# Kernel optimization log

Measured on AMD Instinct MI355X. Metric: run time of the kernel, lower is better.

## Reference

```python
import jax, jax.numpy as jnp
import numpy as np

B = 1024          # number of sessions (graphs)
D = 128           # emb_dim
NH = 4            # num_heads
VOCAB = 50000     # POI vocabulary
NDIST = 512       # distance buckets
MAX_LEN = 160     # max session length


def _lengths():
    # deterministic variable session lengths in [64, 160]
    return np.asarray(64 + (np.arange(B) % 97), dtype=np.int64)


def _layernorm(x, g, b, eps=1e-8):
    mu = x.mean(-1, keepdims=True)
    var = ((x - mu) ** 2).mean(-1, keepdims=True)
    return (x - mu) / jnp.sqrt(var + eps) * g + b


def setup_inputs() -> dict:
    key = jax.random.key(0)
    ks = jax.random.split(key, 16)
    lengths = _lengths()
    N = int(lengths.sum())
    # node -> (graph id, position within graph)
    batch_ids = np.repeat(np.arange(B), lengths)
    node_pos = np.concatenate([np.arange(l) for l in lengths])
    # consecutive (sequence) edges within each session
    starts = np.concatenate([[0], np.cumsum(lengths)[:-1]])
    src = np.concatenate([s + np.arange(l - 1) for s, l in zip(starts, lengths)])
    dst = src + 1
    edge_index = np.stack([src, dst]).astype(np.int64)
    E = edge_index.shape[1]
    s = 1.0 / np.sqrt(D)
    return {
        "POI_embs": jax.random.normal(ks[0], (VOCAB, D), jnp.float32) * 0.02,
        "delta_dis_embs": jax.random.normal(ks[1], (NDIST, D), jnp.float32) * 0.02,
        "att_W": jax.random.normal(ks[2], (D, D), jnp.float32) * s,
        "a_src": jax.random.normal(ks[3], (D,), jnp.float32) * 0.1,
        "a_dst": jax.random.normal(ks[4], (D,), jnp.float32) * 0.1,
        "in_proj_w": jax.random.normal(ks[5], (3 * D, D), jnp.float32) * s,
        "in_proj_b": jnp.zeros((3 * D,), jnp.float32),
        "out_proj_w": jax.random.normal(ks[6], (D, D), jnp.float32) * s,
        "out_proj_b": jnp.zeros((D,), jnp.float32),
        "ln1_g": jnp.ones((D,), jnp.float32), "ln1_b": jnp.zeros((D,), jnp.float32),
        "ln2_g": jnp.ones((D,), jnp.float32), "ln2_b": jnp.zeros((D,), jnp.float32),
        "ffn_w1": jax.random.normal(ks[7], (D, D), jnp.float32) * s,
        "ffn_b1": jnp.zeros((D,), jnp.float32),
        "ffn_w2": jax.random.normal(ks[8], (D, D), jnp.float32) * s,
        "ffn_b2": jnp.zeros((D,), jnp.float32),
        "sess_idx": jax.random.randint(ks[9], (N,), 0, VOCAB),
        "edge_dist": jax.random.randint(ks[10], (E,), 0, NDIST),
        "edge_index": jnp.asarray(edge_index),
        "batch_ids": jnp.asarray(batch_ids),
        "node_pos": jnp.asarray(node_pos),
        "lengths": jnp.asarray(lengths),
    }


def reference(POI_embs, delta_dis_embs, att_W, a_src, a_dst,
              in_proj_w, in_proj_b, out_proj_w, out_proj_b,
              ln1_g, ln1_b, ln2_g, ln2_b,
              ffn_w1, ffn_b1, ffn_w2, ffn_b2,
              sess_idx, edge_dist, edge_index, batch_ids, node_pos, lengths):
    N = sess_idx.shape[0]
    E = edge_index.shape[1]
    # ---- BiSeqGCN: gather -> attention logits -> scatter-softmax -> scatter-add
    x = POI_embs[sess_idx]                    # [N, D] node features
    edge_l = delta_dis_embs[edge_dist]        # [E, D] edge features
    src, dst = edge_index[0], edge_index[1]
    # bidirectional edges: forward (src->dst) then reversed (dst->src)
    j = jnp.concatenate([src, dst])           # message source  x_j
    i = jnp.concatenate([dst, src])           # message target  x_i
    x_i = x[i]                                # [2E, D]
    x_j = x[j]                                # [2E, D]
    fwd_coeff = (x_i[:E] + edge_l) @ att_W.T  # [E, D]
    bwd_coeff = x_i[E:] @ att_W.T             # [E, D]
    logits = jnp.concatenate([fwd_coeff @ a_src, bwd_coeff @ a_dst])  # [2E]
    # scatter-softmax over destination node (torch_geometric softmax, eps=1e-16)
    m = jax.ops.segment_max(logits, i, num_segments=N)
    e = jnp.exp(logits - m[i])
    ssum = jax.ops.segment_sum(e, i, num_segments=N)
    attn = e / (ssum[i] + 1e-16)
    H_u = jax.ops.segment_sum(x_j * attn[:, None], i, num_segments=N)  # [N, D]
    # ---- split/pad to [B, Lmax, D] + padding mask
    Bn = lengths.shape[0]
    pad = jnp.zeros((Bn, MAX_LEN, D), H_u.dtype).at[batch_ids, node_pos].set(H_u)
    mask = jnp.arange(MAX_LEN)[None, :] < lengths[:, None]  # [B, Lmax]
    # ---- MultiheadAttention (Q = LayerNorm(pad); K = V = pad)
    Q = _layernorm(pad, ln1_g, ln1_b)
    Wq, Wk, Wv = jnp.split(in_proj_w, 3, axis=0)
    bq, bk, bv = jnp.split(in_proj_b, 3)
    hd = D // NH
    q = (Q @ Wq.T + bq).reshape(Bn, MAX_LEN, NH, hd)
    k = (pad @ Wk.T + bk).reshape(Bn, MAX_LEN, NH, hd)
    v = (pad @ Wv.T + bv).reshape(Bn, MAX_LEN, NH, hd)
    scores = jnp.einsum('bqhd,bkhd->bhqk', q, k) / jnp.sqrt(jnp.asarray(hd, q.dtype))
    scores = jnp.where(mask[:, None, None, :], scores, -jnp.inf)
    w = jax.nn.softmax(scores, axis=-1)
    ctx = jnp.einsum('bhqk,bkhd->bqhd', w, v).reshape(Bn, MAX_LEN, D)
    out = ctx @ out_proj_w.T + out_proj_b
    out = out + Q
    out = _layernorm(out, ln2_g, ln2_b)
    # ---- PFFN (1x1 convs == per-token linears) with residual
    ffn = jax.nn.relu(out @ ffn_w1.T + ffn_b1) @ ffn_w2.T + ffn_b2
    out = out + ffn
    # ---- masked mean pool over valid positions
    mf = mask[..., None].astype(out.dtype)
    S_u = (out * mf).sum(axis=1) / lengths[:, None].astype(out.dtype)
    return S_u
```

## Files before the change

### kernel.cpp

```cpp
#include <hip/hip_runtime.h>
#include <float.h>


#define D 128
#define NHEAD 4
#define HD 32
#define MAXL 160
#define MAXNK 10
#define VP 168
#define WP 136

typedef __attribute__((ext_vector_type(8))) short short8;
typedef __attribute__((ext_vector_type(4))) float floatx4;

__device__ __forceinline__ float lo2f(unsigned u) {
    union { unsigned i; float f; } x; x.i = u << 16; return x.f;
}
__device__ __forceinline__ float hi2f(unsigned u) {
    union { unsigned i; float f; } x; x.i = u & 0xffff0000u; return x.f;
}
__device__ __forceinline__ unsigned pack2(float a, float b) {
    unsigned r;
    asm("v_cvt_pk_bf16_f32 %0, %1, %2" : "=v"(r) : "v"(a), "v"(b));
    return r;
}
__device__ __forceinline__ unsigned short f2bf(float f) {
    return (unsigned short)pack2(f, 0.f);
}
__device__ __forceinline__ unsigned short f2bfi(float f) {
    union { float f; unsigned i; } x; x.f = f;
    unsigned r = x.i + 0x7fffu + ((x.i >> 16) & 1u);
    return (unsigned short)(r >> 16);
}
__device__ __forceinline__ unsigned pack2i(float a, float b) {
    return (unsigned)f2bfi(a) | ((unsigned)f2bfi(b) << 16);
}
__device__ __forceinline__ float bf2f(unsigned short u) {
    union { unsigned i; float f; } x; x.i = (unsigned)u << 16; return x.f;
}

__launch_bounds__(128)
__global__ void prep1(const float* __restrict__ att_W, const float* __restrict__ a_src,
                      const float* __restrict__ a_dst, const float* __restrict__ in_proj_w,
                      const float* __restrict__ in_proj_b, const float* __restrict__ g1,
                      const float* __restrict__ b1, float* __restrict__ c_src,
                      float* __restrict__ c_dst, float* __restrict__ u, float* __restrict__ z) {
    int p = blockIdx.x;
    int q = threadIdx.x;
    __shared__ float red[4][2];
    float w  = att_W[q * D + p];
    float wq = in_proj_w[p * D + q];
    float s  = a_src[q] * w;
    float d  = a_dst[q] * w;
    float su = g1[q] * wq;
    float sz = b1[q] * wq;
    #pragma unroll
    for (int o = 32; o; o >>= 1) {
        s  += __shfl_down(s, o, 64);
        d  += __shfl_down(d, o, 64);
        su += __shfl_down(su, o, 64);
        sz += __shfl_down(sz, o, 64);
    }
    int wv = q >> 6;
    if ((q & 63) == 0) { red[0][wv] = s; red[1][wv] = d; red[2][wv] = su; red[3][wv] = sz; }
    __syncthreads();
    if (q == 0) {
        c_src[p] = red[0][0] + red[0][1];
        c_dst[p] = red[1][0] + red[1][1];
        u[p]     = red[2][0] + red[2][1];
        z[p]     = red[3][0] + red[3][1] + in_proj_b[p];
    }
}

__global__ void prep2(const float* __restrict__ delta, const float* __restrict__ c_src,
                      const float* __restrict__ in_proj_w, const float* __restrict__ out_proj_w,
                      const float* __restrict__ ffn_w1, const float* __restrict__ ffn_w2,
                      const float* __restrict__ ln1_g, float* __restrict__ tb,
                      unsigned short* __restrict__ wb) {
    int blk = blockIdx.x, t = threadIdx.x;
    if (blk < 128) {
        int b = blk * 4 + (t >> 6);
        int l = t & 63;
        const float* row = delta + (size_t)b * D;
        float s = row[l] * c_src[l] + row[l + 64] * c_src[l + 64];
        #pragma unroll
        for (int o = 32; o; o >>= 1) s += __shfl_down(s, o, 64);
        if (l == 0) tb[b] = s;
    } else {
        int idx = (blk - 128) * 256 + t;
        int m = idx >> 14;
        int within = idx & (D * D - 1);
        float v;
        if (m == 0) v = in_proj_w[within] * ln1_g[within & (D - 1)];
        else if (m == 1) v = in_proj_w[D * D + within];
        else if (m == 2) v = in_proj_w[2 * D * D + within];
        else if (m == 3) v = out_proj_w[within];
        else if (m == 4) v = ffn_w1[within];
        else v = ffn_w2[within];
        wb[idx] = f2bf(v);
    }
}

__launch_bounds__(256)
__global__ void gather_hu(const float* __restrict__ POI, const int* __restrict__ sess_idx,
                          const int* __restrict__ node_pos, const int* __restrict__ batch_ids,
                          const int* __restrict__ edge_dist, const int* __restrict__ lengths,
                          const float* __restrict__ c_src, const float* __restrict__ c_dst,
                          const float* __restrict__ tb, unsigned short* __restrict__ Hu,
                          float* __restrict__ muv, float* __restrict__ rinvv,
                          int* __restrict__ starts, int N) {
    __shared__ unsigned xs[10 * 64];
    __shared__ float s1s[10], s2s[10];
    int R0 = blockIdx.x * 8;
    int t = threadIdx.x;
    int hw = t >> 5, l32 = t & 31;
    float4 cs4 = *(const float4*)(c_src + l32 * 4);
    float4 cd4 = *(const float4*)(c_dst + l32 * 4);
    #pragma unroll
    for (int i = hw; i < 10; i += 8) {
        int n = R0 - 1 + i;
        if (n >= 0 && n < N) {
            int row = sess_idx[n];
            float4 v = *(const float4*)(POI + (size_t)row * D + l32 * 4);
            ((uint2*)(xs + i * 64))[l32] = make_uint2(pack2(v.x, v.y), pack2(v.z, v.w));
            if (i >= 1 && i <= 8) {
                float ps = v.x * cs4.x + v.y * cs4.y + v.z * cs4.z + v.w * cs4.w;
                float pd = v.x * cd4.x + v.y * cd4.y + v.z * cd4.z + v.w * cd4.w;
                #pragma unroll
                for (int o = 16; o; o >>= 1) {
                    ps += __shfl_down(ps, o, 64);
                    pd += __shfl_down(pd, o, 64);
                }
                if (l32 == 0) { s1s[i] = ps; s2s[i] = pd; }
            }
        }
    }
    __syncthreads();
    int j = hw;
    int n = R0 + j;
    if (n >= N) return;
    int g = batch_ids[n], pos = node_pos[n], L = lengths[g];
    bool hasF = pos > 0;
    bool hasB = pos < L - 1;
    float la = hasF ? (s1s[j + 1] + tb[edge_dist[n - 1 - g]]) : -FLT_MAX;
    float lb = hasB ? s2s[j + 1] : -FLT_MAX;
    float m = fmaxf(la, lb);
    float ea = hasF ? __expf(la - m) : 0.f;
    float eb = hasB ? __expf(lb - m) : 0.f;
    float inv = 1.f / (ea + eb + 1e-16f);
    float wa = ea * inv, wb = eb * inv;
    uint2 a = hasF ? ((const uint2*)(xs + j * 64))[l32] : make_uint2(0u, 0u);
    uint2 b = hasB ? ((const uint2*)(xs + (j + 2) * 64))[l32] : make_uint2(0u, 0u);
    float h0 = wa * lo2f(a.x) + wb * lo2f(b.x);
    float h1 = wa * hi2f(a.x) + wb * hi2f(b.x);
    float h2 = wa * lo2f(a.y) + wb * lo2f(b.y);
    float h3 = wa * hi2f(a.y) + wb * hi2f(b.y);
    ((uint2*)Hu)[(size_t)n * 32 + l32] = make_uint2(pack2(h0, h1), pack2(h2, h3));
    float s = h0 + h1 + h2 + h3;
    float ss = h0 * h0 + h1 * h1 + h2 * h2 + h3 * h3;
    #pragma unroll
    for (int o = 1; o < 32; o <<= 1) {
        s += __shfl_xor(s, o, 64);
        ss += __shfl_xor(ss, o, 64);
    }
    if (l32 == 0) {
        float mu = s * (1.f / D);
        float var = ss * (1.f / D) - mu * mu;
        muv[n] = mu;
        rinvv[n] = rsqrtf(var + 1e-8f);
        if (pos == 0) starts[g] = n;
    }
}

__launch_bounds__(256)
__global__ void qkv_split(const unsigned short* __restrict__ Hu, const unsigned short* __restrict__ wb,
                          const float* __restrict__ in_proj_b, const float* __restrict__ u,
                          const float* __restrict__ z, const float* __restrict__ muv,
                          const float* __restrict__ rinvv,
                          unsigned short* __restrict__ qo, unsigned short* __restrict__ ko,
                          unsigned short* __restrict__ vT, int M, int Npad) {
    __shared__ unsigned short Wl[128 * WP];
    int t = threadIdx.x;
    int wv = t >> 6, lane = t & 63;
    int quad = lane >> 4, l16 = lane & 15;
    int r0 = blockIdx.x * 128;
    int rbase = r0 + wv * 32;
    int p = blockIdx.y;
    const float ASCALE = 0.25504364148122793f;
    const unsigned short* W = wb + (p == 0 ? 1 : p == 1 ? 2 : 0) * (D * D);
    for (int i = t; i < 2048; i += 256) {
        int c = i >> 4, kc = (i & 15) * 8;
        *(uint4*)&Wl[c * WP + kc] = *(const uint4*)(W + c * 128 + kc);
    }
    short8 af[2][4];
    #pragma unroll
    for (int mt = 0; mt < 2; mt++) {
        int r = rbase + mt * 16 + l16;
        #pragma unroll
        for (int kk = 0; kk < 4; kk++) {
            if (r < M) af[mt][kk] = *(const short8*)(Hu + (size_t)r * D + kk * 32 + quad * 8);
            else af[mt][kk] = (short8){0, 0, 0, 0, 0, 0, 0, 0};
        }
    }
    __syncthreads();
    floatx4 acc[2][8];
    #pragma unroll
    for (int i = 0; i < 2; i++)
        #pragma unroll
        for (int j = 0; j < 8; j++) acc[i][j] = (floatx4){0.f, 0.f, 0.f, 0.f};
    #pragma unroll
    for (int kk = 0; kk < 4; kk++)
        #pragma unroll
        for (int nt = 0; nt < 8; nt++) {
            short8 bf = *(const short8*)&Wl[(nt * 16 + l16) * WP + kk * 32 + quad * 8];
            acc[0][nt] = __builtin_amdgcn_mfma_f32_16x16x32_bf16(af[0][kk], bf, acc[0][nt], 0, 0, 0);
            acc[1][nt] = __builtin_amdgcn_mfma_f32_16x16x32_bf16(af[1][kk], bf, acc[1][nt], 0, 0, 0);
        }
    __syncthreads();
    if (p == 1) {
        #pragma unroll
        for (int nt = 0; nt < 8; nt++) {
            int col = nt * 16 + l16;
            float bv = in_proj_b[2 * D + col];
            #pragma unroll
            for (int mt = 0; mt < 2; mt++)
                #pragma unroll
                for (int r = 0; r < 4; r += 2) {
                    int ln = wv * 32 + mt * 16 + quad * 4 + r;
                    float v0 = (r0 + ln     < M) ? acc[mt][nt][r]     + bv : 0.f;
                    float v1 = (r0 + ln + 1 < M) ? acc[mt][nt][r + 1] + bv : 0.f;
                    *(unsigned*)&Wl[col * WP + ln] = pack2(v0, v1);
                }
        }
        __syncthreads();
        for (int i = t; i < 2048; i += 256) {
            int col = i >> 4, c8 = (i & 15) * 8;
            *(uint4*)(vT + (size_t)col * Npad + r0 + c8) = *(uint4*)&Wl[col * WP + c8];
        }
    } else {
        if (p == 0) {
            #pragma unroll
            for (int nt = 0; nt < 8; nt++) {
                int col = nt * 16 + l16;
                float bv = in_proj_b[D + col];
                #pragma unroll
                for (int mt = 0; mt < 2; mt++)
                    #pragma unroll
                    for (int r = 0; r < 4; r++)
                        Wl[(wv * 32 + mt * 16 + quad * 4 + r) * WP + col] =
                            f2bf(acc[mt][nt][r] + bv);
            }
        } else {
            float uc[8], zc[8];
            #pragma unroll
            for (int nt = 0; nt < 8; nt++) {
                uc[nt] = u[nt * 16 + l16];
                zc[nt] = z[nt * 16 + l16] * ASCALE;
            }
            #pragma unroll
            for (int mt = 0; mt < 2; mt++)
                #pragma unroll
                for (int r = 0; r < 4; r++) {
                    int ln = wv * 32 + mt * 16 + quad * 4 + r;
                    int grow = r0 + ln;
                    float mr = grow < M ? muv[grow] : 0.f;
                    float rr = (grow < M ? rinvv[grow] : 0.f) * ASCALE;
                    #pragma unroll
                    for (int nt = 0; nt < 8; nt++)
                        Wl[ln * WP + nt * 16 + l16] =
                            f2bf(rr * (acc[mt][nt][r] - mr * uc[nt]) + zc[nt]);
                }
        }
        __syncthreads();
        unsigned short* outp = (p == 0) ? ko : qo;
        for (int i = t; i < 2048; i += 256) {
            int head = i >> 9;
            int j = i & 511;
            int row = j >> 2;
            int c = (j & 3) * 8;
            if (r0 + row < M)
                *(uint4*)(outp + ((size_t)head * Npad + r0 + row) * HD + c) =
                    *(uint4*)&Wl[row * WP + head * 32 + c];
        }
    }
}

__launch_bounds__(128)
__global__ void attn9(const unsigned short* __restrict__ qb,
                      const unsigned short* __restrict__ kb,
                      const unsigned short* __restrict__ vT,
                      const int* __restrict__ starts, const int* __restrict__ lengths,
                      unsigned short* __restrict__ ctx, int Npad) {
    __shared__ unsigned short Vt[HD * VP];
    __shared__ unsigned short Pb[2 * 16 * VP];
    int g = blockIdx.x;
    if (gridDim.x == 1024) {
        int bid = blockIdx.x;
        if (bid < 430) { int r = 96 - bid / 10; g = r + 97 * (bid % 10); }
        else { int b2 = bid - 430; int r = 53 - b2 / 11; g = r + 97 * (b2 % 11); }
    }
    int h = blockIdx.y;
    int start = starts[g], L = lengths[g];
    int t = threadIdx.x;
    int wv = t >> 6, lane = t & 63;
    int l16 = lane & 15, quad = lane >> 4;
    int nk = (L + 15) >> 4;
    int nk2 = (L + 31) >> 5;
    unsigned short* Pw = Pb + wv * 16 * VP;
    if (nk & 1) {
        for (int i = lane; i < 128; i += 64) {
            int row = i >> 3, c = i & 7;
            ((unsigned*)(Pw + row * VP + nk * 16))[c] = 0u;
        }
    }
    int nch = nk2 * 4;
    for (int i = t; i < HD * nch; i += 128) {
        int r = i / nch, c = i - r * nch;
        *(uint4*)&Vt[r * VP + c * 8] =
            *(const uint4*)(vT + (size_t)(h * HD + r) * Npad + start + c * 8);
    }
    const unsigned short* kh = kb + (size_t)h * Npad * HD;
    const unsigned short* qh = qb + (size_t)h * Npad * HD;
    short8 kf[MAXNK];
    #pragma unroll
    for (int kt = 0; kt < MAXNK; kt++) {
        kf[kt] = (short8){0, 0, 0, 0, 0, 0, 0, 0};
        if (kt < nk) {
            int r = kt * 16 + l16;
            if (r < L) kf[kt] = *(const short8*)(kh + (size_t)(start + r) * HD + quad * 8);
        }
    }
    short8 qf[5];
    #pragma unroll
    for (int i = 0; i < 5; i++) {
        qf[i] = (short8){0, 0, 0, 0, 0, 0, 0, 0};
        int qt = wv + 2 * i;
        if (qt < nk) {
            int qrow = qt * 16 + l16;
            if (qrow < L)
                qf[i] = *(const short8*)(qh + (size_t)(start + qrow) * HD + quad * 8);
        }
    }
    __syncthreads();
    #pragma unroll
    for (int i = 0; i < 5; i++) {
        int qt = wv + 2 * i;
        if (qt >= nk) break;
        int q0 = qt * 16;
        floatx4 sacc[MAXNK];
        #pragma unroll
        for (int kt = 0; kt < MAXNK; kt++)
            if (kt < nk)
                sacc[kt] = __builtin_amdgcn_mfma_f32_16x16x32_bf16(
                    kf[kt], qf[i], (floatx4){0.f, 0.f, 0.f, 0.f}, 0, 0, 0);
        float lsum = 0.f;
        #pragma unroll
        for (int kt = 0; kt < MAXNK; kt++)
            if (kt < nk) {
                #pragma unroll
                for (int r = 0; r < 4; r++) {
                    int key = kt * 16 + quad * 4 + r;
                    float p = (key < L) ? __builtin_amdgcn_exp2f(sacc[kt][r]) : 0.f;
                    sacc[kt][r] = p;
                    lsum += p;
                }
                *(uint2*)&Pw[l16 * VP + kt * 16 + quad * 4] =
                    make_uint2(pack2i(sacc[kt][0], sacc[kt][1]),
                               pack2i(sacc[kt][2], sacc[kt][3]));
            }
        lsum += __shfl_xor(lsum, 16);
        lsum += __shfl_xor(lsum, 32);
        float inv = 1.f / lsum;
        #pragma unroll
        for (int nc = 0; nc < 2; nc++) {
            floatx4 oa = (floatx4){0.f, 0.f, 0.f, 0.f};
            floatx4 ob = (floatx4){0.f, 0.f, 0.f, 0.f};
            #pragma unroll
            for (int kc = 0; kc < 5; kc++)
                if (kc < nk2) {
                    short8 pf = *(const short8*)&Pw[l16 * VP + kc * 32 + quad * 8];
                    short8 vf = *(const short8*)&Vt[(nc * 16 + l16) * VP + kc * 32 + quad * 8];
                    if (kc & 1) ob = __builtin_amdgcn_mfma_f32_16x16x32_bf16(pf, vf, ob, 0, 0, 0);
                    else        oa = __builtin_amdgcn_mfma_f32_16x16x32_bf16(pf, vf, oa, 0, 0, 0);
                }
            #pragma unroll
            for (int r = 0; r < 4; r++) {
                int qr = q0 + quad * 4 + r;
                if (qr < L)
                    ctx[(size_t)(start + qr) * D + h * HD + nc * 16 + l16] =
                        f2bfi((oa[r] + ob[r]) * inv);
            }
        }
    }
}

__launch_bounds__(512)
__global__ void tail_fused(const unsigned short* __restrict__ ctx,
                           const unsigned short* __restrict__ Wo,
                           const float* __restrict__ bo,
                           const unsigned short* __restrict__ Hu,
                           const float* __restrict__ muv, const float* __restrict__ rinvv,
                           const float* __restrict__ g1, const float* __restrict__ b1,
                           const float* __restrict__ g2, const float* __restrict__ b2,
                           const unsigned short* __restrict__ W1,
                           const float* __restrict__ b1f,
                           const unsigned short* __restrict__ W2,
                           const float* __restrict__ b2f,
                           const int* __restrict__ batch_ids,
                           const int* __restrict__ lengths,
                           float* __restrict__ out, int M) {
    __shared__ unsigned short Wl[128 * WP];
    __shared__ int gids[128];
    int t = threadIdx.x;
    int wv = t >> 6, lane = t & 63;
    int quad = lane >> 4, l16 = lane & 15;
    int r0 = blockIdx.x * 128;
    int rw = wv * 16;
    int rmax = min(128, M - r0);

    for (int i = t; i < 2048; i += 512) {
        int c = i >> 4, kc = (i & 15) * 8;
        *(uint4*)&Wl[c * WP + kc] = *(const uint4*)(Wo + c * 128 + kc);
    }
    if (t < 128) gids[t] = (r0 + t < M) ? batch_ids[r0 + t] : -1;
    short8 af[4];
    {
        int rA = r0 + rw + l16;
        #pragma unroll
        for (int kk = 0; kk < 4; kk++) {
            if (rA < M) af[kk] = *(const short8*)(ctx + (size_t)rA * D + kk * 32 + quad * 8);
            else af[kk] = (short8){0, 0, 0, 0, 0, 0, 0, 0};
        }
    }
    __syncthreads();
    floatx4 acc[8];
    #pragma unroll
    for (int j = 0; j < 8; j++) acc[j] = (floatx4){0.f, 0.f, 0.f, 0.f};
    #pragma unroll
    for (int kk = 0; kk < 4; kk++)
        #pragma unroll
        for (int nt = 0; nt < 8; nt++) {
            short8 bf = *(const short8*)&Wl[(nt * 16 + l16) * WP + kk * 32 + quad * 8];
            acc[nt] = __builtin_amdgcn_mfma_f32_16x16x32_bf16(af[kk], bf, acc[nt], 0, 0, 0);
        }
    __syncthreads();

    for (int i = t; i < 2048; i += 512) {
        int row = i >> 4, c8 = (i & 15) * 8;
        uint4 hv = make_uint4(0u, 0u, 0u, 0u);
        if (r0 + row < M) hv = *(const uint4*)(Hu + (size_t)(r0 + row) * D + c8);
        *(uint4*)&Wl[row * WP + c8] = hv;
    }
    __syncthreads();
    {
        float g1c[8], b1c[8], boc[8], g2c[8], b2c[8];
        #pragma unroll
        for (int nt = 0; nt < 8; nt++) {
            int col = nt * 16 + l16;
            g1c[nt] = g1[col]; b1c[nt] = b1[col]; boc[nt] = bo[col];
            g2c[nt] = g2[col]; b2c[nt] = b2[col];
        }
        #pragma unroll
        for (int r = 0; r < 4; r++) {
            int lrow = rw + quad * 4 + r;
            int grow = r0 + lrow;
            bool ok = grow < M;
            float mr = ok ? muv[grow] : 0.f;
            float rr = ok ? rinvv[grow] : 0.f;
            float vv[8];
            float s = 0.f, ss = 0.f;
            #pragma unroll
            for (int nt = 0; nt < 8; nt++) {
                float huv = bf2f(Wl[lrow * WP + nt * 16 + l16]);
                float qv = (huv - mr) * rr * g1c[nt] + b1c[nt];
                float v = acc[nt][r] + boc[nt] + qv;
                vv[nt] = v;
                s += v; ss += v * v;
            }
            #pragma unroll
            for (int o = 1; o < 16; o <<= 1) {
                s += __shfl_xor(s, o, 64);
                ss += __shfl_xor(ss, o, 64);
            }
            float mu = s * (1.f / D);
            float var = ss * (1.f / D) - mu * mu;
            float rinv = rsqrtf(var + 1e-8f);
            #pragma unroll
            for (int nt = 0; nt < 8; nt++)
                Wl[lrow * WP + nt * 16 + l16] =
                    f2bf((vv[nt] - mu) * rinv * g2c[nt] + b2c[nt]);
        }
    }
    short8 af2[4];
    #pragma unroll
    for (int kk = 0; kk < 4; kk++)
        af2[kk] = *(const short8*)&Wl[(rw + l16) * WP + kk * 32 + quad * 8];
    __syncthreads();

    {
        int d = t & 127, qt = t >> 7;
        int rlo = qt * 32, rhi = min(rlo + 32, rmax);
        float sum = 0.f;
        int cur = (rlo < rmax) ? gids[rlo] : -1;
        for (int row = rlo; row < rhi; row++) {
            int g = gids[row];
            if (g != cur) {
                atomicAdd(out + (size_t)cur * D + d, sum / (float)lengths[cur]);
                sum = 0.f; cur = g;
            }
            sum += bf2f(Wl[row * WP + d]);
        }
        if (cur >= 0) atomicAdd(out + (size_t)cur * D + d, sum / (float)lengths[cur]);
    }
    __syncthreads();

    for (int i = t; i < 2048; i += 512) {
        int c = i >> 4, kc = (i & 15) * 8;
        *(uint4*)&Wl[c * WP + kc] = *(const uint4*)(W1 + c * 128 + kc);
    }
    __syncthreads();
    #pragma unroll
    for (int j = 0; j < 8; j++) acc[j] = (floatx4){0.f, 0.f, 0.f, 0.f};
    #pragma unroll
    for (int kk = 0; kk < 4; kk++)
        #pragma unroll
        for (int nt = 0; nt < 8; nt++) {
            short8 bf = *(const short8*)&Wl[(nt * 16 + l16) * WP + kk * 32 + quad * 8];
            acc[nt] = __builtin_amdgcn_mfma_f32_16x16x32_bf16(af2[kk], bf, acc[nt], 0, 0, 0);
        }
    __syncthreads();
    #pragma unroll
    for (int nt = 0; nt < 8; nt++) {
        int col = nt * 16 + l16;
        float bv = b1f[col];
        #pragma unroll
        for (int r = 0; r < 4; r++)
            Wl[(rw + quad * 4 + r) * WP + col] = f2bf(fmaxf(acc[nt][r] + bv, 0.f));
    }
    short8 af3[4];
    #pragma unroll
    for (int kk = 0; kk < 4; kk++)
        af3[kk] = *(const short8*)&Wl[(rw + l16) * WP + kk * 32 + quad * 8];
    __syncthreads();

    for (int i = t; i < 2048; i += 512) {
        int c = i >> 4, kc = (i & 15) * 8;
        *(uint4*)&Wl[c * WP + kc] = *(const uint4*)(W2 + c * 128 + kc);
    }
    __syncthreads();
    #pragma unroll
    for (int j = 0; j < 8; j++) acc[j] = (floatx4){0.f, 0.f, 0.f, 0.f};
    #pragma unroll
    for (int kk = 0; kk < 4; kk++)
        #pragma unroll
        for (int nt = 0; nt < 8; nt++) {
            short8 bf = *(const short8*)&Wl[(nt * 16 + l16) * WP + kk * 32 + quad * 8];
            acc[nt] = __builtin_amdgcn_mfma_f32_16x16x32_bf16(af3[kk], bf, acc[nt], 0, 0, 0);
        }
    __syncthreads();
    #pragma unroll
    for (int nt = 0; nt < 8; nt++) {
        int col = nt * 16 + l16;
        float bv = b2f[col];
        #pragma unroll
        for (int r = 0; r < 4; r++)
            Wl[(rw + quad * 4 + r) * WP + col] = f2bf(acc[nt][r] + bv);
    }
    __syncthreads();
    {
        int d = t & 127, qt = t >> 7;
        int rlo = qt * 32, rhi = min(rlo + 32, rmax);
        float sum = 0.f;
        int cur = (rlo < rmax) ? gids[rlo] : -1;
        for (int row = rlo; row < rhi; row++) {
            int g = gids[row];
            if (g != cur) {
                atomicAdd(out + (size_t)cur * D + d, sum / (float)lengths[cur]);
                sum = 0.f; cur = g;
            }
            sum += bf2f(Wl[row * WP + d]);
        }
        if (cur >= 0) atomicAdd(out + (size_t)cur * D + d, sum / (float)lengths[cur]);
    }
}

extern "C" void kernel_launch(void* const* d_in, const int* in_sizes, int n_in,
                              void* d_out, int out_size, void* d_ws, size_t ws_size,
                              hipStream_t stream) {
    const float* POI        = (const float*)d_in[0];
    const float* delta      = (const float*)d_in[1];
    const float* att_W      = (const float*)d_in[2];
    const float* a_src      = (const float*)d_in[3];
    const float* a_dst      = (const float*)d_in[4];
    const float* in_proj_w  = (const float*)d_in[5];
    const float* in_proj_b  = (const float*)d_in[6];
    const float* out_proj_w = (const float*)d_in[7];
    const float* out_proj_b = (const float*)d_in[8];
    const float* ln1_g      = (const float*)d_in[9];
    const float* ln1_b      = (const float*)d_in[10];
    const float* ln2_g      = (const float*)d_in[11];
    const float* ln2_b      = (const float*)d_in[12];
    const float* ffn_w1     = (const float*)d_in[13];
    const float* ffn_b1     = (const float*)d_in[14];
    const float* ffn_w2     = (const float*)d_in[15];
    const float* ffn_b2     = (const float*)d_in[16];
    const int* sess_idx     = (const int*)d_in[17];
    const int* edge_dist    = (const int*)d_in[18];
    const int* batch_ids    = (const int*)d_in[20];
    const int* node_pos     = (const int*)d_in[21];
    const int* lengths      = (const int*)d_in[22];

    int N = in_sizes[17];
    int B = in_sizes[22];
    int gb = (N + 127) / 128;
    int Npad = gb * 128;

    char* base = (char*)d_ws;
    size_t off = 0;
    auto alloc = [&](size_t bytes) { size_t c = off; off = (off + bytes + 255) & ~(size_t)255; return c; };
    size_t o_csrc  = alloc(D * 4);
    size_t o_cdst  = alloc(D * 4);
    size_t o_t     = alloc(512 * 4);
    size_t o_start = alloc((size_t)B * 4);
    size_t o_mu    = alloc((size_t)N * 4);
    size_t o_ri    = alloc((size_t)N * 4);
    size_t o_u     = alloc(D * 4);
    size_t o_z     = alloc(D * 4);
    size_t o_wb    = alloc(6 * D * D * 2);
    size_t nb      = (size_t)Npad * D * 2;
    size_t o_A = alloc(nb);
    size_t o_B = alloc(nb);
    size_t o_C = alloc(nb);
    size_t o_D = alloc(nb);
    if (ws_size < off) return;

    float* c_src = (float*)(base + o_csrc);
    float* c_dst = (float*)(base + o_cdst);
    float* tb    = (float*)(base + o_t);
    int*   starts = (int*)(base + o_start);
    float* muv   = (float*)(base + o_mu);
    float* rinvv = (float*)(base + o_ri);
    float* u     = (float*)(base + o_u);
    float* z     = (float*)(base + o_z);
    unsigned short* wb = (unsigned short*)(base + o_wb);
    unsigned short* bufA = (unsigned short*)(base + o_A);
    unsigned short* bufB = (unsigned short*)(base + o_B);
    unsigned short* bufC = (unsigned short*)(base + o_C);
    unsigned short* bufD = (unsigned short*)(base + o_D);

    hipMemsetAsync(d_out, 0, (size_t)B * D * 4, stream);
    prep1<<<128, 128, 0, stream>>>(att_W, a_src, a_dst, in_proj_w, in_proj_b,
                                   ln1_g, ln1_b, c_src, c_dst, u, z);
    prep2<<<512, 256, 0, stream>>>(delta, c_src, in_proj_w, out_proj_w,
                                   ffn_w1, ffn_w2, ln1_g, tb, wb);
    gather_hu<<<(N + 7) / 8, 256, 0, stream>>>(POI, sess_idx, node_pos, batch_ids,
                                               edge_dist, lengths, c_src, c_dst, tb,
                                               bufB, muv, rinvv, starts, N);

    qkv_split<<<dim3(gb, 3), 256, 0, stream>>>(bufB, wb, in_proj_b, u, z, muv, rinvv,
                                               bufC, bufD, bufA, N, Npad);

    attn9<<<dim3(B, NHEAD), 128, 0, stream>>>(bufC, bufD, bufA, starts, lengths, bufC, Npad);

    tail_fused<<<gb, 512, 0, stream>>>(bufC, wb + 3 * D * D, out_proj_b, bufB, muv, rinvv,
                                       ln1_g, ln1_b, ln2_g, ln2_b,
                                       wb + 4 * D * D, ffn_b1, wb + 5 * D * D, ffn_b2,
                                       batch_ids, lengths, (float*)d_out, N);
}
```

Before: 279.4 us.

## Read MLP weight fragments directly from global memory, drop LDS staging and barriers

The post-attention kernel no longer stages the out-projection, FFN W1 and W2 weight matrices into shared memory. Each wave now loads its MFMA B fragments straight from global memory, which is L2-resident because every block reads the same 32KB matrices. Each wave also loads only its own 16 rows of H_u into LDS, so several block-wide barriers can be removed. The cost is more global and L2 traffic per wave with uncoalesced short8 loads, plus more exposed load latency before each MFMA.

```diff
diff --git a/kernel.cpp b/kernel.cpp
--- a/kernel.cpp
+++ b/kernel.cpp
@@ -418,11 +418,8 @@
     int rw = wv * 16;
     int rmax = min(128, M - r0);
 
-    for (int i = t; i < 2048; i += 512) {
-        int c = i >> 4, kc = (i & 15) * 8;
-        *(uint4*)&Wl[c * WP + kc] = *(const uint4*)(Wo + c * 128 + kc);
-    }
     if (t < 128) gids[t] = (r0 + t < M) ? batch_ids[r0 + t] : -1;
+
     short8 af[4];
     {
         int rA = r0 + rw + l16;
@@ -432,26 +429,25 @@
             else af[kk] = (short8){0, 0, 0, 0, 0, 0, 0, 0};
         }
     }
-    __syncthreads();
-    floatx4 acc[8];
-    #pragma unroll
-    for (int j = 0; j < 8; j++) acc[j] = (floatx4){0.f, 0.f, 0.f, 0.f};
-    #pragma unroll
-    for (int kk = 0; kk < 4; kk++)
-        #pragma unroll
-        for (int nt = 0; nt < 8; nt++) {
-            short8 bf = *(const short8*)&Wl[(nt * 16 + l16) * WP + kk * 32 + quad * 8];
-            acc[nt] = __builtin_amdgcn_mfma_f32_16x16x32_bf16(af[kk], bf, acc[nt], 0, 0, 0);
-        }
-    __syncthreads();
-
-    for (int i = t; i < 2048; i += 512) {
-        int row = i >> 4, c8 = (i & 15) * 8;
+    for (int j = lane; j < 256; j += 64) {
+        int row = rw + (j >> 4);
+        int c8 = (j & 15) * 8;
         uint4 hv = make_uint4(0u, 0u, 0u, 0u);
         if (r0 + row < M) hv = *(const uint4*)(Hu + (size_t)(r0 + row) * D + c8);
         *(uint4*)&Wl[row * WP + c8] = hv;
     }
-    __syncthreads();
+
+    floatx4 acc[8];
+    #pragma unroll
+    for (int j = 0; j < 8; j++) acc[j] = (floatx4){0.f, 0.f, 0.f, 0.f};
+    #pragma unroll
+    for (int kk = 0; kk < 4; kk++)
+        #pragma unroll
+        for (int nt = 0; nt < 8; nt++) {
+            short8 bf = *(const short8*)(Wo + (size_t)(nt * 16 + l16) * D + kk * 32 + quad * 8);
+            acc[nt] = __builtin_amdgcn_mfma_f32_16x16x32_bf16(af[kk], bf, acc[nt], 0, 0, 0);
+        }
+
     {
         float g1c[8], b1c[8], boc[8], g2c[8], b2c[8];
         #pragma unroll
@@ -514,21 +510,15 @@
     }
     __syncthreads();
 
-    for (int i = t; i < 2048; i += 512) {
-        int c = i >> 4, kc = (i & 15) * 8;
-        *(uint4*)&Wl[c * WP + kc] = *(const uint4*)(W1 + c * 128 + kc);
-    }
-    __syncthreads();
     #pragma unroll
     for (int j = 0; j < 8; j++) acc[j] = (floatx4){0.f, 0.f, 0.f, 0.f};
     #pragma unroll
     for (int kk = 0; kk < 4; kk++)
         #pragma unroll
         for (int nt = 0; nt < 8; nt++) {
-            short8 bf = *(const short8*)&Wl[(nt * 16 + l16) * WP + kk * 32 + quad * 8];
+            short8 bf = *(const short8*)(W1 + (size_t)(nt * 16 + l16) * D + kk * 32 + quad * 8);
             acc[nt] = __builtin_amdgcn_mfma_f32_16x16x32_bf16(af2[kk], bf, acc[nt], 0, 0, 0);
         }
-    __syncthreads();
     #pragma unroll
     for (int nt = 0; nt < 8; nt++) {
         int col = nt * 16 + l16;
@@ -541,23 +531,16 @@
     #pragma unroll
     for (int kk = 0; kk < 4; kk++)
         af3[kk] = *(const short8*)&Wl[(rw + l16) * WP + kk * 32 + quad * 8];
-    __syncthreads();
-
-    for (int i = t; i < 2048; i += 512) {
-        int c = i >> 4, kc = (i & 15) * 8;
-        *(uint4*)&Wl[c * WP + kc] = *(const uint4*)(W2 + c * 128 + kc);
-    }
-    __syncthreads();
+
     #pragma unroll
     for (int j = 0; j < 8; j++) acc[j] = (floatx4){0.f, 0.f, 0.f, 0.f};
     #pragma unroll
     for (int kk = 0; kk < 4; kk++)
         #pragma unroll
         for (int nt = 0; nt < 8; nt++) {
-            short8 bf = *(const short8*)&Wl[(nt * 16 + l16) * WP + kk * 32 + quad * 8];
+            short8 bf = *(const short8*)(W2 + (size_t)(nt * 16 + l16) * D + kk * 32 + quad * 8);
             acc[nt] = __builtin_amdgcn_mfma_f32_16x16x32_bf16(af3[kk], bf, acc[nt], 0, 0, 0);
         }
-    __syncthreads();
     #pragma unroll
     for (int nt = 0; nt < 8; nt++) {
         int col = nt * 16 + l16;
@@ -567,6 +550,7 @@
             Wl[(rw + quad * 4 + r) * WP + col] = f2bf(acc[nt][r] + bv);
     }
     __syncthreads();
+
     {
         int d = t & 127, qt = t >> 7;
         int rlo = qt * 32, rhi = min(rlo + 32, rmax);
```

After: 333.1 us. 1.19x slower.
